# Optimization experiments

Hardware: AMD Instinct MI355X
Metric: run time of the kernel (lower is better)

The kernel has to match this reference:

```python
import jax, jax.numpy as jnp
import numpy as np

EMBED_DIM = 2048
NUM_HEADS = 16
NUM_HEADS_KV = 16
HEAD_DIM = EMBED_DIM // NUM_HEADS  # 128
ROT_DIM = HEAD_DIM // 2            # rotary_emb_dim = 64 (partial rotary)
ROPE_BASE = 10000.0
SEQLEN = 2048


def _rope_cos_sin(seqlen):
    # inv_freq over rotary dim (fp32 positions, as pos_idx_in_fp32=True)
    inv_freq = 1.0 / (ROPE_BASE ** (jnp.arange(0, ROT_DIM, 2, dtype=jnp.float32) / ROT_DIM))
    t = jnp.arange(seqlen, dtype=jnp.float32)
    freqs = jnp.outer(t, inv_freq)                 # (S, ROT_DIM//2)
    return jnp.cos(freqs), jnp.sin(freqs)


def _apply_rotary(x, cos, sin):
    # x: (B, S, H, D); non-interleaved (GPT-NeoX) rotary on first ROT_DIM dims
    rd = cos.shape[-1] * 2
    x_rot, x_pass = x[..., :rd], x[..., rd:]
    x1, x2 = x_rot[..., : rd // 2], x_rot[..., rd // 2 :]
    c = cos[None, :, None, :]
    s = sin[None, :, None, :]
    o1 = x1 * c - x2 * s
    o2 = x1 * s + x2 * c
    return jnp.concatenate([o1, o2, x_pass], axis=-1)


def setup_inputs() -> dict:
    key = jax.random.key(0)
    ks = jax.random.split(key, 5)
    scale_in = 1.0 / np.sqrt(EMBED_DIM)
    return {
        "x_q": jax.random.normal(ks[0], (SEQLEN, EMBED_DIM), dtype=jnp.float32),
        "Wqkv_w": jax.random.normal(ks[1], (HEAD_DIM * (NUM_HEADS + 2 * NUM_HEADS_KV), EMBED_DIM), dtype=jnp.float32) * scale_in,
        "Wqkv_b": jax.random.normal(ks[2], (HEAD_DIM * (NUM_HEADS + 2 * NUM_HEADS_KV),), dtype=jnp.float32) * 0.01,
        "Wo_w": jax.random.normal(ks[3], (EMBED_DIM, EMBED_DIM), dtype=jnp.float32) * scale_in,
        "Wo_b": jax.random.normal(ks[4], (EMBED_DIM,), dtype=jnp.float32) * 0.01,
    }


def reference(x_q, Wqkv_w, Wqkv_b, Wo_w, Wo_b):
    S = x_q.shape[0]
    H, Hkv, D = NUM_HEADS, NUM_HEADS_KV, HEAD_DIM
    # fused QKV projection
    qkv = x_q @ Wqkv_w.T + Wqkv_b                     # (S, (H+2Hkv)*D)
    q = qkv[:, : H * D].reshape(1, S, H, D)
    kv = qkv[:, H * D :].reshape(1, S, 2, Hkv, D)
    # rotary (q_position_ids = k_position_ids = arange(S))
    cos, sin = _rope_cos_sin(S)
    q = _apply_rotary(q, cos, sin)
    k = _apply_rotary(kv[:, :, 0], cos, sin)          # (1, S, Hkv, D)
    v = kv[:, :, 1]
    # causal attention, softmax scale 1/sqrt(D)
    scores = jnp.einsum("bshd,bthd->bhst", q, k) / jnp.sqrt(jnp.float32(D))
    causal = jnp.arange(S)[:, None] >= jnp.arange(S)[None, :]  # (S, S)
    scores = jnp.where(causal[None, None], scores, jnp.float32(-1e30))
    attn = jax.nn.softmax(scores, axis=-1)
    out = jnp.einsum("bhst,bthd->bshd", attn, v)      # (1, S, H, D)
    out = out.reshape(1, S, H * D)
    out = out @ Wo_w.T + Wo_b
    return out[0]                                     # (S, E)
```

## Files before the change

kernel.cpp:

```cpp
#include <hip/hip_runtime.h>
#include <stdint.h>

#define QKV_N 6144
#define ATT_SCALE 0.08838834764831845f

typedef __attribute__((ext_vector_type(8))) short short8;
typedef __attribute__((ext_vector_type(4))) float f32x4;

__device__ __forceinline__ uint16_t f2b(float x){
  uint32_t u = __float_as_uint(x);
  uint32_t r = (u + 0x7fffu + ((u >> 16) & 1u)) >> 16;
  return (uint16_t)r;
}
__device__ __forceinline__ float b2f(uint16_t h){
  return __uint_as_float(((uint32_t)h) << 16);
}
__device__ __forceinline__ void g2l16(const void* g, void* l){
  __builtin_amdgcn_global_load_lds((const __attribute__((address_space(1))) void*)g,
                                   (__attribute__((address_space(3))) void*)l, 16, 0, 0);
}

__device__ __forceinline__ void cvt8(const float* __restrict__ in, uint16_t* __restrict__ out, int i){
  const float4* p = (const float4*)in;
  float4 a = p[2*i], b = p[2*i+1];
  union { short8 v; uint16_t u[8]; } o;
  o.u[0]=f2b(a.x); o.u[1]=f2b(a.y); o.u[2]=f2b(a.z); o.u[3]=f2b(a.w);
  o.u[4]=f2b(b.x); o.u[5]=f2b(b.y); o.u[6]=f2b(b.z); o.u[7]=f2b(b.w);
  ((short8*)out)[i] = o.v;
}

__global__ __launch_bounds__(256) void k_prep(const float* __restrict__ x,
                                              const float* __restrict__ wqkv,
                                              const float* __restrict__ wo,
                                              uint16_t* __restrict__ xb,
                                              uint16_t* __restrict__ wqkvb,
                                              uint16_t* __restrict__ wob,
                                              float* __restrict__ ct,
                                              float* __restrict__ st){
  const int b = blockIdx.x, tid = threadIdx.x;
  if (b < 2048) {
    cvt8(x, xb, b*256 + tid);
  } else if (b < 8192) {
    cvt8(wqkv, wqkvb, (b - 2048)*256 + tid);
  } else if (b < 10240) {
    cvt8(wo, wob, (b - 8192)*256 + tid);
  } else {
    int i = (b - 10240)*256 + tid;
    int s = i >> 5, d = i & 31;
    float inv = __expf(-(float)d * (9.210340371976184f / 32.0f));
    float f = (float)s * inv;
    ct[i] = cosf(f);
    st[i] = sinf(f);
  }
}

__global__ __launch_bounds__(512, 1) void k_gemmA(const uint16_t* __restrict__ A,
                                                  const uint16_t* __restrict__ B,
                                                  const float* __restrict__ bias,
                                                  uint16_t* __restrict__ C){
  __shared__ uint16_t As[3*4096];
  __shared__ uint16_t Bs[3*6144];
  const int K = 2048, N = 6144;

  const int wg = blockIdx.x;
  const int xcd = wg & 7, bi = wg >> 3;
  const int m0 = (xcd*2 + (bi & 1)) * 128;
  const int n0 = (bi >> 1) * 192;

  const int tid = threadIdx.x;
  const int wid = tid >> 6, l = tid & 63;
  const int wm = wid >> 2, wn = wid & 3;
  const int g = l >> 4, c = l & 15;

  const int rpA = tid >> 3, sA = (tid & 7) ^ (rpA & 7);
  const size_t srcA0 = (size_t)(m0 + rpA*2 + (sA >> 2)) * K + (sA & 3) * 8;
  const size_t srcB0 = (size_t)(n0 + rpA*2 + (sA >> 2)) * K + (sA & 3) * 8;
  const int rpB2 = 64 + (tid >> 3), sB2 = (tid & 7) ^ (rpB2 & 7);
  const size_t srcB1 = (size_t)(n0 + rpB2*2 + (sB2 >> 2)) * K + (sB2 & 3) * 8;

  const int pg   = ((c & 1) << 2) | g;
  const int slb  = (pg ^ ((c >> 1) & 7)) << 3;
  const int rpa0 = wm*32 + (c >> 1);
  const int rpb0 = wn*24 + (c >> 1);

  f32x4 acc[4][3] = {};
  const int NT = K >> 5;

  #pragma unroll
  for (int t0 = 0; t0 < 2; ++t0) {
    g2l16(A + srcA0 + t0*32, (void*)(As + t0*4096 + tid*8));
    g2l16(B + srcB0 + t0*32, (void*)(Bs + t0*6144 + tid*8));
    if (tid < 256)
      g2l16(B + srcB1 + t0*32, (void*)(Bs + t0*6144 + 4096 + tid*8));
  }
  if (wid < 4) { asm volatile("s_waitcnt vmcnt(3)" ::: "memory"); }
  else         { asm volatile("s_waitcnt vmcnt(2)" ::: "memory"); }
  __builtin_amdgcn_s_barrier();

  #pragma unroll 3
  for (int t = 0; t < NT; ++t) {
    const uint16_t* __restrict__ Ab = As + (t % 3)*4096;
    const uint16_t* __restrict__ Bb = Bs + (t % 3)*6144;
    const int t2 = t + 2;

    short8 av[4], bv[3];
    #pragma unroll
    for (int mi = 0; mi < 4; ++mi)
      av[mi] = *(const short8*)&Ab[(rpa0 + mi*8)*64 + slb];
    #pragma unroll
    for (int ni = 0; ni < 3; ++ni)
      bv[ni] = *(const short8*)&Bb[(rpb0 + ni*8)*64 + slb];
    if (t2 < NT) {
      const int b2 = (t2 % 3);
      g2l16(A + srcA0 + t2*32, (void*)(As + b2*4096 + tid*8));
      g2l16(B + srcB0 + t2*32, (void*)(Bs + b2*6144 + tid*8));
      if (tid < 256)
        g2l16(B + srcB1 + t2*32, (void*)(Bs + b2*6144 + 4096 + tid*8));
    }
    __builtin_amdgcn_s_barrier();
    __builtin_amdgcn_s_setprio(1);
    #pragma unroll
    for (int mi = 0; mi < 4; ++mi)
      #pragma unroll
      for (int ni = 0; ni < 3; ++ni)
        acc[mi][ni] = __builtin_amdgcn_mfma_f32_16x16x32_bf16(av[mi], bv[ni], acc[mi][ni], 0, 0, 0);
    __builtin_amdgcn_s_setprio(0);
    if (wid < 4) { asm volatile("s_waitcnt vmcnt(3)" ::: "memory"); }
    else         { asm volatile("s_waitcnt vmcnt(2)" ::: "memory"); }
    __builtin_amdgcn_s_barrier();
  }

  #pragma unroll
  for (int ni = 0; ni < 3; ++ni) {
    const int col = n0 + wn*48 + ni*16 + c;
    const float bvl = bias[col];
    #pragma unroll
    for (int mi = 0; mi < 4; ++mi) {
      const int row0 = m0 + wm*64 + mi*16 + g*4;
      #pragma unroll
      for (int j = 0; j < 4; ++j)
        C[(size_t)(row0 + j)*N + col] = f2b(acc[mi][ni][j] + bvl);
    }
  }
}

__global__ __launch_bounds__(512, 1) void k_gemm128(const uint16_t* __restrict__ A,
                                                    const uint16_t* __restrict__ B,
                                                    const float* __restrict__ bias,
                                                    float* __restrict__ C,
                                                    int M, int N, int K){
  __shared__ uint16_t As[4*4096];
  __shared__ uint16_t Bs[4*4096];

  const int wg = blockIdx.x;
  const int xcd = wg & 7, bi = wg >> 3;
  const int m0 = (xcd*2 + (bi & 1)) * 128;
  const int n0 = (bi >> 1) * 128;

  const int tid = threadIdx.x;
  const int wid = tid >> 6, l = tid & 63;
  const int wm = wid >> 2, wn = wid & 3;
  const int g = l >> 4, c = l & 15;

  const int rp_s = tid >> 3, q_s = tid & 7, s_s = q_s ^ (rp_s & 7);
  const int srcA = (m0 + rp_s*2 + (s_s >> 2)) * K + (s_s & 3) * 8;
  const int srcB = (n0 + rp_s*2 + (s_s >> 2)) * K + (s_s & 3) * 8;

  const int pg  = ((c & 1) << 2) | g;
  const int slb = (pg ^ ((c >> 1) & 7)) << 3;
  const int ra0 = wm*32 + (c >> 1);
  const int rb0 = wn*16 + (c >> 1);

  f32x4 acc[4][2] = {};
  const int NT = K >> 5;

  #pragma unroll
  for (int t0 = 0; t0 < 3; ++t0) {
    g2l16(A + srcA + t0*32, (void*)(As + t0*4096 + tid*8));
    g2l16(B + srcB + t0*32, (void*)(Bs + t0*4096 + tid*8));
  }
  asm volatile("s_waitcnt vmcnt(4)" ::: "memory");
  __builtin_amdgcn_s_barrier();

  #pragma unroll 4
  for (int t = 0; t < NT; ++t) {
    const uint16_t* __restrict__ Ab = As + (t & 3)*4096;
    const uint16_t* __restrict__ Bb = Bs + (t & 3)*4096;
    const int t3 = t + 3;
    const int b3 = (t3 & 3)*4096;

    short8 av[4], bv[2];
    #pragma unroll
    for (int mi = 0; mi < 4; ++mi)
      av[mi] = *(const short8*)&Ab[(ra0 + mi*8)*64 + slb];
    #pragma unroll
    for (int ni = 0; ni < 2; ++ni)
      bv[ni] = *(const short8*)&Bb[(rb0 + ni*8)*64 + slb];
    if (t3 < NT) {
      g2l16(A + srcA + t3*32, (void*)(As + b3 + tid*8));
      g2l16(B + srcB + t3*32, (void*)(Bs + b3 + tid*8));
    }
    __builtin_amdgcn_s_barrier();
    __builtin_amdgcn_s_setprio(1);
    #pragma unroll
    for (int mi = 0; mi < 4; ++mi)
      #pragma unroll
      for (int ni = 0; ni < 2; ++ni)
        acc[mi][ni] = __builtin_amdgcn_mfma_f32_16x16x32_bf16(av[mi], bv[ni], acc[mi][ni], 0, 0, 0);
    __builtin_amdgcn_s_setprio(0);
    asm volatile("s_waitcnt vmcnt(4)" ::: "memory");
    __builtin_amdgcn_s_barrier();
  }

  #pragma unroll
  for (int ni = 0; ni < 2; ++ni) {
    const int col = n0 + wn*32 + ni*16 + c;
    const float bvl = bias[col];
    #pragma unroll
    for (int mi = 0; mi < 4; ++mi) {
      const int row0 = m0 + wm*64 + mi*16 + g*4;
      #pragma unroll
      for (int j = 0; j < 4; ++j)
        C[(size_t)(row0 + j)*N + col] = acc[mi][ni][j] + bvl;
    }
  }
}

__global__ __launch_bounds__(256) void k_rope_vt(const uint16_t* __restrict__ qkv,
                                                 const float* __restrict__ ct,
                                                 const float* __restrict__ st,
                                                 uint16_t* __restrict__ qo,
                                                 uint16_t* __restrict__ ko,
                                                 uint16_t* __restrict__ vt){
  const int blk = blockIdx.x, tid = threadIdx.x;
  if (blk < 4096) {
    int idx = blk * 256 + tid;
    int db = idx & 15;
    int s  = (idx >> 4) & 2047;
    int h  = (idx >> 15) & 15;
    int which = idx >> 19;
    const uint16_t* src = qkv + (size_t)s * QKV_N + which * 2048 + h * 128;
    uint16_t* dst = (which ? ko : qo) + (((size_t)(h*2048 + s)) << 7) + db*8;
    const float scale = which ? 1.0f : ATT_SCALE;
    int d0 = db * 8;
    union { short8 v; uint16_t u[8]; } o;
    if (d0 >= 64) {
      short8 xv = *(const short8*)(src + d0);
      #pragma unroll
      for (int e = 0; e < 8; ++e) o.u[e] = f2b(b2f((uint16_t)xv[e]) * scale);
    } else {
      int dd = d0 & 31;
      short8 a = *(const short8*)(src + dd);
      short8 b = *(const short8*)(src + dd + 32);
      float4 c0 = *(const float4*)(ct + s*32 + dd);
      float4 c1 = *(const float4*)(ct + s*32 + dd + 4);
      float4 s0 = *(const float4*)(st + s*32 + dd);
      float4 s1 = *(const float4*)(st + s*32 + dd + 4);
      float cc[8] = {c0.x,c0.y,c0.z,c0.w,c1.x,c1.y,c1.z,c1.w};
      float ss[8] = {s0.x,s0.y,s0.z,s0.w,s1.x,s1.y,s1.z,s1.w};
      #pragma unroll
      for (int e = 0; e < 8; ++e) {
        float x1 = b2f((uint16_t)a[e]), x2 = b2f((uint16_t)b[e]);
        float v = (d0 < 32) ? (x1*cc[e] - x2*ss[e]) : (x1*ss[e] + x2*cc[e]);
        o.u[e] = f2b(v * scale);
      }
    }
    *(short8*)dst = o.v;
  } else {
    __shared__ uint16_t tl[64][80];
    const int b = blk - 4096;
    const int st_ = b & 31, dt = (b >> 5) & 1, h = b >> 6;
    const int s_l = tid >> 2, cch = (tid & 3) * 16;
    const uint16_t* src = qkv + (size_t)(st_*64 + s_l) * QKV_N + 4096 + h*128 + dt*64 + cch;
    short8 a = *(const short8*)src;
    short8 b2 = *(const short8*)(src + 8);
    #pragma unroll
    for (int e = 0; e < 8; ++e) {
      tl[cch + e][s_l]     = (uint16_t)a[e];
      tl[cch + 8 + e][s_l] = (uint16_t)b2[e];
    }
    __syncthreads();
    const int d_l = tid >> 2;
    uint16_t* dst = vt + ((size_t)h << 18) + (size_t)(dt*64 + d_l) * 2048 + st_*64 + cch;
    *(short8*)dst       = *(const short8*)&tl[d_l][cch];
    *(short8*)(dst + 8) = *(const short8*)&tl[d_l][cch + 8];
  }
}

__global__ __launch_bounds__(512, 1) void k_attn(const uint16_t* __restrict__ Q,
                                                 const uint16_t* __restrict__ Kb,
                                                 const uint16_t* __restrict__ Vtg,
                                                 uint16_t* __restrict__ Out){
  __shared__ uint16_t Ks[2][2][64*128];
  __shared__ uint16_t Vs[2][2][128*64];
  __shared__ uint16_t Ps[8][16*88];

  const int bid = blockIdx.x;
  const int lin = (bid & 7) * 32 + (bid >> 3);
  const int h = lin >> 4;
  const int pair = lin & 15;

  const int tid = threadIdx.x, w = tid >> 6, l = tid & 63;
  const int gid = w >> 2, wq = w & 3;
  const int tg = tid & 255;
  const int g = l >> 4, c = l & 15;
  const int swz = (c & 7) << 4;

  const uint16_t* __restrict__ Qh = Q   + ((size_t)h << 18);
  const uint16_t* __restrict__ Kh = Kb  + ((size_t)h << 18);
  const uint16_t* __restrict__ Vh = Vtg + ((size_t)h << 18);
  float* scratch = (float*)&Ks[0][0][0];

  int koff[4], voff[4];
  #pragma unroll
  for (int j = 0; j < 4; ++j) {
    int kr = j*16 + (tg >> 4);
    koff[j] = kr*128 + (((tg & 15) ^ (kr & 7)) << 3);
    int vd = j*32 + (tg >> 3);
    voff[j] = vd*2048 + (((tg & 7) ^ (vd & 7)) << 3);
  }

  uint16_t* KsG = &Ks[gid][0][0];
  uint16_t* VsG = &Vs[gid][0][0];

  #pragma unroll 1
  for (int half = 0; half < 2; ++half) {
    const int qt = half ? (31 - pair) : pair;
    const int nt = qt + 1;
    const int nsteps = (nt + 1) >> 1;
    const int qrow = qt*64 + wq*16 + c;

    short8 qf[4];
    #pragma unroll
    for (int t = 0; t < 4; ++t)
      qf[t] = *(const short8*)&Qh[(size_t)qrow*128 + t*32 + g*8];

    f32x4 acc[8] = {};
    float mrow[4], lsum[4];
    #pragma unroll
    for (int j = 0; j < 4; ++j) { mrow[j] = -3e38f; lsum[j] = 0.0f; }

    if (gid < nt) {
      #pragma unroll
      for (int j = 0; j < 4; ++j) {
        g2l16(Kh + (size_t)gid*8192 + koff[j], (void*)(KsG + j*2048 + tg*8));
        g2l16(Vh + gid*64 + voff[j],           (void*)(VsG + j*2048 + tg*8));
      }
    }
    asm volatile("s_waitcnt vmcnt(0)" ::: "memory");
    __syncthreads();

    #pragma unroll 1
    for (int step = 0; step < nsteps; ++step) {
      const int kt = 2*step + gid;
      const int cur = step & 1;
      if (kt + 2 < nt) {
        const int k1 = kt + 2;
        #pragma unroll
        for (int j = 0; j < 4; ++j) {
          g2l16(Kh + (size_t)k1*8192 + koff[j], (void*)(KsG + (cur^1)*8192 + j*2048 + tg*8));
          g2l16(Vh + k1*64 + voff[j],           (void*)(VsG + (cur^1)*8192 + j*2048 + tg*8));
        }
      }

      if (kt < nt) {
        const int k0 = kt * 64;
        const uint16_t* Kcur = KsG + cur*8192;
        const uint16_t* Vcur = VsG + cur*8192;

        f32x4 sc4[4] = {};
        __builtin_amdgcn_s_setprio(1);
        #pragma unroll
        for (int ct2 = 0; ct2 < 4; ++ct2) {
          const char* krp = (const char*)Kcur + (ct2*16 + c)*256;
          #pragma unroll
          for (int t = 0; t < 4; ++t) {
            short8 kb = *(const short8*)(krp + ((t*64 + g*16) ^ swz));
            sc4[ct2] = __builtin_amdgcn_mfma_f32_16x16x32_bf16(qf[t], kb, sc4[ct2], 0, 0, 0);
          }
        }
        __builtin_amdgcn_s_setprio(0);

        const bool lastt = (kt == nt - 1);
        float va[4][4];
        float m4[4];
        int fastok = 1;
        #pragma unroll
        for (int j = 0; j < 4; ++j) {
          const int qg = qt*64 + wq*16 + g*4 + j;
          float v0 = sc4[0][j], v1 = sc4[1][j], v2 = sc4[2][j], v3 = sc4[3][j];
          if (lastt) {
            if (k0 +      c > qg) v0 = -3e38f;
            if (k0 + 16 + c > qg) v1 = -3e38f;
            if (k0 + 32 + c > qg) v2 = -3e38f;
            if (k0 + 48 + c > qg) v3 = -3e38f;
          }
          va[j][0] = v0; va[j][1] = v1; va[j][2] = v2; va[j][3] = v3;
          float m = fmaxf(fmaxf(fmaxf(v0, v1), v2), v3);
          m4[j] = m;
          fastok &= (m <= mrow[j] + 8.0f) ? 1 : 0;
        }
        if (__all(fastok)) {
          #pragma unroll
          for (int j = 0; j < 4; ++j) {
            const float mj = mrow[j];
            const float p0 = __expf(va[j][0] - mj), p1 = __expf(va[j][1] - mj),
                        p2 = __expf(va[j][2] - mj), p3 = __expf(va[j][3] - mj);
            lsum[j] += (p0 + p1) + (p2 + p3);
            uint16_t* pw = &Ps[w][(g*4 + j)*88];
            pw[c] = f2b(p0); pw[16+c] = f2b(p1); pw[32+c] = f2b(p2); pw[48+c] = f2b(p3);
          }
        } else {
          #pragma unroll
          for (int j = 0; j < 4; ++j) {
            float t0 = m4[j];
            #pragma unroll
            for (int d2 = 1; d2 < 16; d2 <<= 1) t0 = fmaxf(t0, __shfl_xor(t0, d2, 64));
            const float mn = fmaxf(mrow[j], t0);
            const float scl = __expf(mrow[j] - mn);
            const float p0 = __expf(va[j][0] - mn), p1 = __expf(va[j][1] - mn),
                        p2 = __expf(va[j][2] - mn), p3 = __expf(va[j][3] - mn);
            lsum[j] = lsum[j]*scl + (p0 + p1) + (p2 + p3);
            mrow[j] = mn;
            #pragma unroll
            for (int n = 0; n < 8; ++n) acc[n][j] *= scl;
            uint16_t* pw = &Ps[w][(g*4 + j)*88];
            pw[c] = f2b(p0); pw[16+c] = f2b(p1); pw[32+c] = f2b(p2); pw[48+c] = f2b(p3);
          }
        }

        __builtin_amdgcn_s_setprio(1);
        #pragma unroll
        for (int kk = 0; kk < 2; ++kk) {
          short8 pf = *(const short8*)&Ps[w][c*88 + kk*32 + g*8];
          #pragma unroll
          for (int n = 0; n < 8; ++n) {
            const char* vrp = (const char*)Vcur + (n*16 + c)*128;
            short8 vf = *(const short8*)(vrp + ((kk*64 + g*16) ^ swz));
            acc[n] = __builtin_amdgcn_mfma_f32_16x16x32_bf16(pf, vf, acc[n], 0, 0, 0);
          }
        }
        __builtin_amdgcn_s_setprio(0);
      }

      asm volatile("s_waitcnt vmcnt(0)" ::: "memory");
      __syncthreads();
    }

    float lrow[4];
    #pragma unroll
    for (int j = 0; j < 4; ++j) {
      float rs = lsum[j];
      #pragma unroll
      for (int d2 = 1; d2 < 16; d2 <<= 1) rs += __shfl_xor(rs, d2, 64);
      lrow[j] = rs;
    }

    float* Up = scratch + wq * 2112;
    if (gid == 1) {
      #pragma unroll
      for (int j = 0; j < 4; ++j) {
        const int row = g*4 + j;
        #pragma unroll
        for (int n = 0; n < 8; ++n)
          Up[row*128 + n*16 + c] = acc[n][j];
        if (c == 0) { Up[2048 + row] = mrow[j]; Up[2064 + row] = lrow[j]; }
      }
    }
    __syncthreads();
    if (gid == 0) {
      #pragma unroll
      for (int j = 0; j < 4; ++j) {
        const int row = g*4 + j;
        const int qg = qt*64 + wq*16 + row;
        const float mB = Up[2048 + row], lB = Up[2064 + row];
        const float mn = fmaxf(mrow[j], mB);
        const float e1 = __expf(mrow[j] - mn);
        const float e2 = __expf(mB - mn);
        const float inv = 1.0f / (lrow[j]*e1 + lB*e2);
        #pragma unroll
        for (int n = 0; n < 8; ++n) {
          const float u = acc[n][j]*e1 + Up[row*128 + n*16 + c]*e2;
          Out[(size_t)qg*2048 + h*128 + n*16 + c] = f2b(u * inv);
        }
      }
    }
    __syncthreads();
  }
}

extern "C" void kernel_launch(void* const* d_in, const int* in_sizes, int n_in,
                              void* d_out, int out_size, void* d_ws, size_t ws_size,
                              hipStream_t stream){
  const float* x    = (const float*)d_in[0];
  const float* Wqkv = (const float*)d_in[1];
  const float* bqkv = (const float*)d_in[2];
  const float* Wo   = (const float*)d_in[3];
  const float* bo   = (const float*)d_in[4];

  char* ws = (char*)d_ws;
  uint16_t* q_bf    = (uint16_t*)(ws);
  uint16_t* k_bf    = (uint16_t*)(ws + 8388608);
  uint16_t* vt_bf   = (uint16_t*)(ws + 16777216);
  uint16_t* attn_bf = (uint16_t*)(ws + 25165824);
  uint16_t* x_bf    = attn_bf;
  uint16_t* wqkv_bf = (uint16_t*)(ws + 33554432);
  uint16_t* wo_bf   = (uint16_t*)(ws + 58720256);
  uint16_t* qkv_bf  = (uint16_t*)(ws + 67108864);
  float*    cos_t   = (float*)(ws + 92274688);
  float*    sin_t   = (float*)(ws + 92536832);

  k_prep<<<dim3(10496), dim3(256), 0, stream>>>(x, Wqkv, Wo, x_bf, wqkv_bf, wo_bf,
                                                cos_t, sin_t);
  k_gemmA<<<dim3(512), dim3(512), 0, stream>>>(x_bf, wqkv_bf, bqkv, qkv_bf);
  k_rope_vt<<<dim3(5120), dim3(256), 0, stream>>>(qkv_bf, cos_t, sin_t, q_bf, k_bf, vt_bf);
  k_attn<<<dim3(256), dim3(512), 0, stream>>>(q_bf, k_bf, vt_bf, attn_bf);
  k_gemm128<<<dim3(256), dim3(512), 0, stream>>>(attn_bf, wo_bf, bo, (float*)d_out,
                                                 2048, 2048, 2048);
}
```

Measured before the change: 165.2 us.

## Enlarge QKV GEMM tiles to 256x256 with quadrant-split double-buffered pipeline

```diff
diff --git a/kernel.cpp b/kernel.cpp
--- a/kernel.cpp
+++ b/kernel.cpp
@@ -58,85 +58,150 @@
                                                   const uint16_t* __restrict__ B,
                                                   const float* __restrict__ bias,
                                                   uint16_t* __restrict__ C){
-  __shared__ uint16_t As[3*4096];
-  __shared__ uint16_t Bs[3*6144];
+  __shared__ uint16_t As[2*16384];
+  __shared__ uint16_t Bs[2*16384];
   const int K = 2048, N = 6144;
 
   const int wg = blockIdx.x;
-  const int xcd = wg & 7, bi = wg >> 3;
-  const int m0 = (xcd*2 + (bi & 1)) * 128;
-  const int n0 = (bi >> 1) * 192;
+  const int xcd = wg & 7, ib = wg >> 3;
+  const int m0 = (ib / 3) * 256;
+  const int n0 = (xcd * 3 + (ib % 3)) * 256;
 
   const int tid = threadIdx.x;
   const int wid = tid >> 6, l = tid & 63;
   const int wm = wid >> 2, wn = wid & 3;
   const int g = l >> 4, c = l & 15;
 
-  const int rpA = tid >> 3, sA = (tid & 7) ^ (rpA & 7);
-  const size_t srcA0 = (size_t)(m0 + rpA*2 + (sA >> 2)) * K + (sA & 3) * 8;
-  const size_t srcB0 = (size_t)(n0 + rpA*2 + (sA >> 2)) * K + (sA & 3) * 8;
-  const int rpB2 = 64 + (tid >> 3), sB2 = (tid & 7) ^ (rpB2 & 7);
-  const size_t srcB1 = (size_t)(n0 + rpB2*2 + (sB2 >> 2)) * K + (sB2 & 3) * 8;
-
-  const int pg   = ((c & 1) << 2) | g;
-  const int slb  = (pg ^ ((c >> 1) & 7)) << 3;
-  const int rpa0 = wm*32 + (c >> 1);
-  const int rpb0 = wn*24 + (c >> 1);
-
-  f32x4 acc[4][3] = {};
-  const int NT = K >> 5;
-
+  const int srow = tid >> 3, sq = tid & 7;
+  const int scol = (sq ^ (srow & 7)) * 8;
+  size_t srcA[2][2], srcB[2][2];
   #pragma unroll
-  for (int t0 = 0; t0 < 2; ++t0) {
-    g2l16(A + srcA0 + t0*32, (void*)(As + t0*4096 + tid*8));
-    g2l16(B + srcB0 + t0*32, (void*)(Bs + t0*6144 + tid*8));
-    if (tid < 256)
-      g2l16(B + srcB1 + t0*32, (void*)(Bs + t0*6144 + 4096 + tid*8));
-  }
-  if (wid < 4) { asm volatile("s_waitcnt vmcnt(3)" ::: "memory"); }
-  else         { asm volatile("s_waitcnt vmcnt(2)" ::: "memory"); }
+  for (int hf = 0; hf < 2; ++hf)
+    #pragma unroll
+    for (int r = 0; r < 2; ++r) {
+      srcA[hf][r] = (size_t)(m0 + hf*128 + r*64 + srow) * K + scol;
+      srcB[hf][r] = (size_t)(n0 + hf*128 + r*64 + srow) * K + scol;
+    }
+
+  const int sl0 = ((g)     ^ (c & 7)) << 3;
+  const int sl1 = ((4 | g) ^ (c & 7)) << 3;
+  const int arb = (wm*128 + c) * 64;
+  const int brb = (wn*64  + c) * 64;
+
+  f32x4 acc[8][4] = {};
+  const int NT = K >> 6;
+
+  #pragma unroll
+  for (int t0 = 0; t0 < 2; ++t0)
+    #pragma unroll
+    for (int hf = 0; hf < 2; ++hf)
+      #pragma unroll
+      for (int r = 0; r < 2; ++r) {
+        g2l16(A + srcA[hf][r] + t0*64, (void*)(As + t0*16384 + hf*8192 + r*4096 + tid*8));
+        g2l16(B + srcB[hf][r] + t0*64, (void*)(Bs + t0*16384 + hf*8192 + r*4096 + tid*8));
+      }
+  asm volatile("s_waitcnt vmcnt(8)" ::: "memory");
   __builtin_amdgcn_s_barrier();
 
-  #pragma unroll 3
   for (int t = 0; t < NT; ++t) {
-    const uint16_t* __restrict__ Ab = As + (t % 3)*4096;
-    const uint16_t* __restrict__ Bb = Bs + (t % 3)*6144;
-    const int t2 = t + 2;
-
-    short8 av[4], bv[3];
+    const int cur = t & 1;
+    const uint16_t* __restrict__ Ab = As + cur*16384;
+    const uint16_t* __restrict__ Bb = Bs + cur*16384;
+    const bool pf = (t + 2) < NT;
+    const size_t ko = (size_t)(t + 2) * 64;
+    short8 a1[8], b0[4], b1[4], a2[8];
+
+    #pragma unroll
+    for (int mi = 0; mi < 4; ++mi) {
+      a1[mi*2]   = *(const short8*)&Ab[arb + mi*1024 + sl0];
+      a1[mi*2+1] = *(const short8*)&Ab[arb + mi*1024 + sl1];
+    }
+    #pragma unroll
+    for (int ni = 0; ni < 2; ++ni) {
+      b0[ni*2]   = *(const short8*)&Bb[brb + ni*1024 + sl0];
+      b0[ni*2+1] = *(const short8*)&Bb[brb + ni*1024 + sl1];
+    }
+    __builtin_amdgcn_s_barrier();
+    __builtin_amdgcn_s_setprio(1);
     #pragma unroll
     for (int mi = 0; mi < 4; ++mi)
-      av[mi] = *(const short8*)&Ab[(rpa0 + mi*8)*64 + slb];
-    #pragma unroll
-    for (int ni = 0; ni < 3; ++ni)
-      bv[ni] = *(const short8*)&Bb[(rpb0 + ni*8)*64 + slb];
-    if (t2 < NT) {
-      const int b2 = (t2 % 3);
-      g2l16(A + srcA0 + t2*32, (void*)(As + b2*4096 + tid*8));
-      g2l16(B + srcB0 + t2*32, (void*)(Bs + b2*6144 + tid*8));
-      if (tid < 256)
-        g2l16(B + srcB1 + t2*32, (void*)(Bs + b2*6144 + 4096 + tid*8));
+      #pragma unroll
+      for (int ni = 0; ni < 2; ++ni)
+        #pragma unroll
+        for (int kk = 0; kk < 2; ++kk)
+          acc[mi][ni] = __builtin_amdgcn_mfma_f32_16x16x32_bf16(a1[mi*2+kk], b0[ni*2+kk], acc[mi][ni], 0, 0, 0);
+    __builtin_amdgcn_s_setprio(0);
+    __builtin_amdgcn_s_barrier();
+
+    #pragma unroll
+    for (int ni = 0; ni < 2; ++ni) {
+      b1[ni*2]   = *(const short8*)&Bb[brb + (ni+2)*1024 + sl0];
+      b1[ni*2+1] = *(const short8*)&Bb[brb + (ni+2)*1024 + sl1];
     }
     __builtin_amdgcn_s_barrier();
     __builtin_amdgcn_s_setprio(1);
     #pragma unroll
     for (int mi = 0; mi < 4; ++mi)
       #pragma unroll
-      for (int ni = 0; ni < 3; ++ni)
-        acc[mi][ni] = __builtin_amdgcn_mfma_f32_16x16x32_bf16(av[mi], bv[ni], acc[mi][ni], 0, 0, 0);
+      for (int ni = 0; ni < 2; ++ni)
+        #pragma unroll
+        for (int kk = 0; kk < 2; ++kk)
+          acc[mi][ni+2] = __builtin_amdgcn_mfma_f32_16x16x32_bf16(a1[mi*2+kk], b1[ni*2+kk], acc[mi][ni+2], 0, 0, 0);
     __builtin_amdgcn_s_setprio(0);
-    if (wid < 4) { asm volatile("s_waitcnt vmcnt(3)" ::: "memory"); }
-    else         { asm volatile("s_waitcnt vmcnt(2)" ::: "memory"); }
+    __builtin_amdgcn_s_barrier();
+
+    if (pf) {
+      #pragma unroll
+      for (int hf = 0; hf < 2; ++hf)
+        #pragma unroll
+        for (int r = 0; r < 2; ++r)
+          g2l16(B + srcB[hf][r] + ko, (void*)(Bs + cur*16384 + hf*8192 + r*4096 + tid*8));
+    }
+    #pragma unroll
+    for (int mi = 0; mi < 4; ++mi) {
+      a2[mi*2]   = *(const short8*)&Ab[arb + (mi+4)*1024 + sl0];
+      a2[mi*2+1] = *(const short8*)&Ab[arb + (mi+4)*1024 + sl1];
+    }
+    __builtin_amdgcn_s_barrier();
+    __builtin_amdgcn_s_setprio(1);
+    #pragma unroll
+    for (int mi = 0; mi < 4; ++mi)
+      #pragma unroll
+      for (int ni = 0; ni < 2; ++ni)
+        #pragma unroll
+        for (int kk = 0; kk < 2; ++kk)
+          acc[mi+4][ni+2] = __builtin_amdgcn_mfma_f32_16x16x32_bf16(a2[mi*2+kk], b1[ni*2+kk], acc[mi+4][ni+2], 0, 0, 0);
+    __builtin_amdgcn_s_setprio(0);
+    __builtin_amdgcn_s_barrier();
+
+    if (pf) {
+      #pragma unroll
+      for (int hf = 0; hf < 2; ++hf)
+        #pragma unroll
+        for (int r = 0; r < 2; ++r)
+          g2l16(A + srcA[hf][r] + ko, (void*)(As + cur*16384 + hf*8192 + r*4096 + tid*8));
+    }
+    __builtin_amdgcn_s_setprio(1);
+    #pragma unroll
+    for (int mi = 0; mi < 4; ++mi)
+      #pragma unroll
+      for (int ni = 0; ni < 2; ++ni)
+        #pragma unroll
+        for (int kk = 0; kk < 2; ++kk)
+          acc[mi+4][ni] = __builtin_amdgcn_mfma_f32_16x16x32_bf16(a2[mi*2+kk], b0[ni*2+kk], acc[mi+4][ni], 0, 0, 0);
+    __builtin_amdgcn_s_setprio(0);
+    if (pf) { asm volatile("s_waitcnt vmcnt(8)" ::: "memory"); }
+    else    { asm volatile("s_waitcnt vmcnt(0)" ::: "memory"); }
     __builtin_amdgcn_s_barrier();
   }
 
   #pragma unroll
-  for (int ni = 0; ni < 3; ++ni) {
-    const int col = n0 + wn*48 + ni*16 + c;
+  for (int ni = 0; ni < 4; ++ni) {
+    const int col = n0 + wn*64 + ni*16 + c;
     const float bvl = bias[col];
     #pragma unroll
-    for (int mi = 0; mi < 4; ++mi) {
-      const int row0 = m0 + wm*64 + mi*16 + g*4;
+    for (int mi = 0; mi < 8; ++mi) {
+      const int row0 = m0 + wm*128 + mi*16 + g*4;
       #pragma unroll
       for (int j = 0; j < 4; ++j)
         C[(size_t)(row0 + j)*N + col] = f2b(acc[mi][ni][j] + bvl);
@@ -512,7 +577,7 @@
 
   k_prep<<<dim3(10496), dim3(256), 0, stream>>>(x, Wqkv, Wo, x_bf, wqkv_bf, wo_bf,
                                                 cos_t, sin_t);
-  k_gemmA<<<dim3(512), dim3(512), 0, stream>>>(x_bf, wqkv_bf, bqkv, qkv_bf);
+  k_gemmA<<<dim3(192), dim3(512), 0, stream>>>(x_bf, wqkv_bf, bqkv, qkv_bf);
   k_rope_vt<<<dim3(5120), dim3(256), 0, stream>>>(qkv_bf, cos_t, sin_t, q_bf, k_bf, vt_bf);
   k_attn<<<dim3(256), dim3(512), 0, stream>>>(q_bf, k_bf, vt_bf, attn_bf);
   k_gemm128<<<dim3(256), dim3(512), 0, stream>>>(attn_bf, wo_bf, bo, (float*)d_out,
```

Result: no change. 165.9 us (+0.5%).

## Split attention into one block per query tile with 32-wide KV tiles

Applied to the files above, without the earlier changes.

```diff
diff --git a/kernel.cpp b/kernel.cpp
--- a/kernel.cpp
+++ b/kernel.cpp
@@ -287,18 +287,18 @@
   }
 }
 
-__global__ __launch_bounds__(512, 1) void k_attn(const uint16_t* __restrict__ Q,
+__global__ __launch_bounds__(512, 4) void k_attn(const uint16_t* __restrict__ Q,
                                                  const uint16_t* __restrict__ Kb,
                                                  const uint16_t* __restrict__ Vtg,
                                                  uint16_t* __restrict__ Out){
-  __shared__ uint16_t Ks[2][2][64*128];
-  __shared__ uint16_t Vs[2][2][128*64];
-  __shared__ uint16_t Ps[8][16*88];
+  __shared__ uint16_t Ks[2][2][32*128];
+  __shared__ uint16_t Vs[2][2][128*32];
+  __shared__ uint16_t Ps[8][16*40];
 
   const int bid = blockIdx.x;
-  const int lin = (bid & 7) * 32 + (bid >> 3);
-  const int h = lin >> 4;
-  const int pair = lin & 15;
+  const int xcd = bid & 7, r = bid >> 3;
+  const int h = 2*xcd + (r & 1);
+  const int qt = (r < 32) ? (r >> 1) : (31 - ((r - 32) >> 1));
 
   const int tid = threadIdx.x, w = tid >> 6, l = tid & 63;
   const int gid = w >> 2, wq = w & 3;
@@ -311,181 +311,166 @@
   const uint16_t* __restrict__ Vh = Vtg + ((size_t)h << 18);
   float* scratch = (float*)&Ks[0][0][0];
 
-  int koff[4], voff[4];
-  #pragma unroll
-  for (int j = 0; j < 4; ++j) {
+  int koff[2], voff[2];
+  #pragma unroll
+  for (int j = 0; j < 2; ++j) {
     int kr = j*16 + (tg >> 4);
     koff[j] = kr*128 + (((tg & 15) ^ (kr & 7)) << 3);
-    int vd = j*32 + (tg >> 3);
-    voff[j] = vd*2048 + (((tg & 7) ^ (vd & 7)) << 3);
+    int vd = j*64 + (tg >> 2);
+    voff[j] = vd*2048 + (((tg & 3) ^ (vd & 3)) << 3);
   }
 
   uint16_t* KsG = &Ks[gid][0][0];
   uint16_t* VsG = &Vs[gid][0][0];
 
+  const int nt = (qt + 1) * 2;
+  const int nsteps = nt >> 1;
+  const int qrow = qt*64 + wq*16 + c;
+
+  short8 qf[4];
+  #pragma unroll
+  for (int t = 0; t < 4; ++t)
+    qf[t] = *(const short8*)&Qh[(size_t)qrow*128 + t*32 + g*8];
+
+  f32x4 acc[8] = {};
+  float mrow[4], lsum[4];
+  #pragma unroll
+  for (int j = 0; j < 4; ++j) { mrow[j] = -3e38f; lsum[j] = 0.0f; }
+
+  #pragma unroll
+  for (int j = 0; j < 2; ++j) {
+    g2l16(Kh + (size_t)gid*4096 + koff[j], (void*)(KsG + j*2048 + tg*8));
+    g2l16(Vh + gid*32 + voff[j],           (void*)(VsG + j*2048 + tg*8));
+  }
+  asm volatile("s_waitcnt vmcnt(0)" ::: "memory");
+  __syncthreads();
+
   #pragma unroll 1
-  for (int half = 0; half < 2; ++half) {
-    const int qt = half ? (31 - pair) : pair;
-    const int nt = qt + 1;
-    const int nsteps = (nt + 1) >> 1;
-    const int qrow = qt*64 + wq*16 + c;
-
-    short8 qf[4];
-    #pragma unroll
-    for (int t = 0; t < 4; ++t)
-      qf[t] = *(const short8*)&Qh[(size_t)qrow*128 + t*32 + g*8];
-
-    f32x4 acc[8] = {};
-    float mrow[4], lsum[4];
-    #pragma unroll
-    for (int j = 0; j < 4; ++j) { mrow[j] = -3e38f; lsum[j] = 0.0f; }
-
-    if (gid < nt) {
+  for (int step = 0; step < nsteps; ++step) {
+    const int kt = 2*step + gid;
+    const int cur = step & 1;
+    if (kt + 2 < nt) {
+      const int k1 = kt + 2;
+      #pragma unroll
+      for (int j = 0; j < 2; ++j) {
+        g2l16(Kh + (size_t)k1*4096 + koff[j], (void*)(KsG + (cur^1)*4096 + j*2048 + tg*8));
+        g2l16(Vh + k1*32 + voff[j],           (void*)(VsG + (cur^1)*4096 + j*2048 + tg*8));
+      }
+    }
+
+    {
+      const int k0 = kt * 32;
+      const uint16_t* Kcur = KsG + cur*4096;
+      const uint16_t* Vcur = VsG + cur*4096;
+
+      f32x4 sc2[2] = {};
+      __builtin_amdgcn_s_setprio(1);
+      #pragma unroll
+      for (int ct2 = 0; ct2 < 2; ++ct2) {
+        const char* krp = (const char*)Kcur + (ct2*16 + c)*256;
+        #pragma unroll
+        for (int t = 0; t < 4; ++t) {
+          short8 kb = *(const short8*)(krp + ((t*64 + g*16) ^ swz));
+          sc2[ct2] = __builtin_amdgcn_mfma_f32_16x16x32_bf16(qf[t], kb, sc2[ct2], 0, 0, 0);
+        }
+      }
+      __builtin_amdgcn_s_setprio(0);
+
+      const bool maskt = (kt >= nt - 2);
+      float m4[4];
+      int fastok = 1;
       #pragma unroll
       for (int j = 0; j < 4; ++j) {
-        g2l16(Kh + (size_t)gid*8192 + koff[j], (void*)(KsG + j*2048 + tg*8));
-        g2l16(Vh + gid*64 + voff[j],           (void*)(VsG + j*2048 + tg*8));
-      }
-    }
+        const int qg = qt*64 + wq*16 + g*4 + j;
+        float v0 = sc2[0][j], v1 = sc2[1][j];
+        if (maskt) {
+          if (k0 +      c > qg) v0 = -3e38f;
+          if (k0 + 16 + c > qg) v1 = -3e38f;
+        }
+        sc2[0][j] = v0; sc2[1][j] = v1;
+        float m = fmaxf(v0, v1);
+        m4[j] = m;
+        fastok &= (m <= mrow[j] + 8.0f) ? 1 : 0;
+      }
+      if (__all(fastok)) {
+        #pragma unroll
+        for (int j = 0; j < 4; ++j) {
+          const float mj = mrow[j];
+          const float p0 = __expf(sc2[0][j] - mj), p1 = __expf(sc2[1][j] - mj);
+          lsum[j] += p0 + p1;
+          uint16_t* pw = &Ps[w][(g*4 + j)*40];
+          pw[c] = f2b(p0); pw[16+c] = f2b(p1);
+        }
+      } else {
+        #pragma unroll
+        for (int j = 0; j < 4; ++j) {
+          float t0 = m4[j];
+          #pragma unroll
+          for (int d2 = 1; d2 < 16; d2 <<= 1) t0 = fmaxf(t0, __shfl_xor(t0, d2, 64));
+          const float mn = fmaxf(mrow[j], t0);
+          const float scl = __expf(mrow[j] - mn);
+          const float p0 = __expf(sc2[0][j] - mn), p1 = __expf(sc2[1][j] - mn);
+          lsum[j] = lsum[j]*scl + p0 + p1;
+          mrow[j] = mn;
+          #pragma unroll
+          for (int n = 0; n < 8; ++n) acc[n][j] *= scl;
+          uint16_t* pw = &Ps[w][(g*4 + j)*40];
+          pw[c] = f2b(p0); pw[16+c] = f2b(p1);
+        }
+      }
+
+      short8 pf = *(const short8*)&Ps[w][c*40 + g*8];
+      __builtin_amdgcn_s_setprio(1);
+      #pragma unroll
+      for (int n = 0; n < 8; ++n) {
+        const char* vrp = (const char*)Vcur + (n*16 + c)*64;
+        short8 vf = *(const short8*)(vrp + ((g*16) ^ (((c & 3)) << 4)));
+        acc[n] = __builtin_amdgcn_mfma_f32_16x16x32_bf16(pf, vf, acc[n], 0, 0, 0);
+      }
+      __builtin_amdgcn_s_setprio(0);
+    }
+
     asm volatile("s_waitcnt vmcnt(0)" ::: "memory");
     __syncthreads();
-
-    #pragma unroll 1
-    for (int step = 0; step < nsteps; ++step) {
-      const int kt = 2*step + gid;
-      const int cur = step & 1;
-      if (kt + 2 < nt) {
-        const int k1 = kt + 2;
-        #pragma unroll
-        for (int j = 0; j < 4; ++j) {
-          g2l16(Kh + (size_t)k1*8192 + koff[j], (void*)(KsG + (cur^1)*8192 + j*2048 + tg*8));
-          g2l16(Vh + k1*64 + voff[j],           (void*)(VsG + (cur^1)*8192 + j*2048 + tg*8));
-        }
-      }
-
-      if (kt < nt) {
-        const int k0 = kt * 64;
-        const uint16_t* Kcur = KsG + cur*8192;
-        const uint16_t* Vcur = VsG + cur*8192;
-
-        f32x4 sc4[4] = {};
-        __builtin_amdgcn_s_setprio(1);
-        #pragma unroll
-        for (int ct2 = 0; ct2 < 4; ++ct2) {
-          const char* krp = (const char*)Kcur + (ct2*16 + c)*256;
-          #pragma unroll
-          for (int t = 0; t < 4; ++t) {
-            short8 kb = *(const short8*)(krp + ((t*64 + g*16) ^ swz));
-            sc4[ct2] = __builtin_amdgcn_mfma_f32_16x16x32_bf16(qf[t], kb, sc4[ct2], 0, 0, 0);
-          }
-        }
-        __builtin_amdgcn_s_setprio(0);
-
-        const bool lastt = (kt == nt - 1);
-        float va[4][4];
-        float m4[4];
-        int fastok = 1;
-        #pragma unroll
-        for (int j = 0; j < 4; ++j) {
-          const int qg = qt*64 + wq*16 + g*4 + j;
-          float v0 = sc4[0][j], v1 = sc4[1][j], v2 = sc4[2][j], v3 = sc4[3][j];
-          if (lastt) {
-            if (k0 +      c > qg) v0 = -3e38f;
-            if (k0 + 16 + c > qg) v1 = -3e38f;
-            if (k0 + 32 + c > qg) v2 = -3e38f;
-            if (k0 + 48 + c > qg) v3 = -3e38f;
-          }
-          va[j][0] = v0; va[j][1] = v1; va[j][2] = v2; va[j][3] = v3;
-          float m = fmaxf(fmaxf(fmaxf(v0, v1), v2), v3);
-          m4[j] = m;
-          fastok &= (m <= mrow[j] + 8.0f) ? 1 : 0;
-        }
-        if (__all(fastok)) {
-          #pragma unroll
-          for (int j = 0; j < 4; ++j) {
-            const float mj = mrow[j];
-            const float p0 = __expf(va[j][0] - mj), p1 = __expf(va[j][1] - mj),
-                        p2 = __expf(va[j][2] - mj), p3 = __expf(va[j][3] - mj);
-            lsum[j] += (p0 + p1) + (p2 + p3);
-            uint16_t* pw = &Ps[w][(g*4 + j)*88];
-            pw[c] = f2b(p0); pw[16+c] = f2b(p1); pw[32+c] = f2b(p2); pw[48+c] = f2b(p3);
-          }
-        } else {
-          #pragma unroll
-          for (int j = 0; j < 4; ++j) {
-            float t0 = m4[j];
-            #pragma unroll
-            for (int d2 = 1; d2 < 16; d2 <<= 1) t0 = fmaxf(t0, __shfl_xor(t0, d2, 64));
-            const float mn = fmaxf(mrow[j], t0);
-            const float scl = __expf(mrow[j] - mn);
-            const float p0 = __expf(va[j][0] - mn), p1 = __expf(va[j][1] - mn),
-                        p2 = __expf(va[j][2] - mn), p3 = __expf(va[j][3] - mn);
-            lsum[j] = lsum[j]*scl + (p0 + p1) + (p2 + p3);
-            mrow[j] = mn;
-            #pragma unroll
-            for (int n = 0; n < 8; ++n) acc[n][j] *= scl;
-            uint16_t* pw = &Ps[w][(g*4 + j)*88];
-            pw[c] = f2b(p0); pw[16+c] = f2b(p1); pw[32+c] = f2b(p2); pw[48+c] = f2b(p3);
-          }
-        }
-
-        __builtin_amdgcn_s_setprio(1);
-        #pragma unroll
-        for (int kk = 0; kk < 2; ++kk) {
-          short8 pf = *(const short8*)&Ps[w][c*88 + kk*32 + g*8];
-          #pragma unroll
-          for (int n = 0; n < 8; ++n) {
-            const char* vrp = (const char*)Vcur + (n*16 + c)*128;
-            short8 vf = *(const short8*)(vrp + ((kk*64 + g*16) ^ swz));
-            acc[n] = __builtin_amdgcn_mfma_f32_16x16x32_bf16(pf, vf, acc[n], 0, 0, 0);
-          }
-        }
-        __builtin_amdgcn_s_setprio(0);
-      }
-
-      asm volatile("s_waitcnt vmcnt(0)" ::: "memory");
-      __syncthreads();
-    }
-
-    float lrow[4];
+  }
+
+  float lrow[4];
+  #pragma unroll
+  for (int j = 0; j < 4; ++j) {
+    float rs = lsum[j];
+    #pragma unroll
+    for (int d2 = 1; d2 < 16; d2 <<= 1) rs += __shfl_xor(rs, d2, 64);
+    lrow[j] = rs;
+  }
+
+  float* Up = scratch + wq * 2112;
+  if (gid == 1) {
     #pragma unroll
     for (int j = 0; j < 4; ++j) {
-      float rs = lsum[j];
-      #pragma unroll
-      for (int d2 = 1; d2 < 16; d2 <<= 1) rs += __shfl_xor(rs, d2, 64);
-      lrow[j] = rs;
-    }
-
-    float* Up = scratch + wq * 2112;
-    if (gid == 1) {
-      #pragma unroll
-      for (int j = 0; j < 4; ++j) {
-        const int row = g*4 + j;
-        #pragma unroll
-        for (int n = 0; n < 8; ++n)
-          Up[row*128 + n*16 + c] = acc[n][j];
-        if (c == 0) { Up[2048 + row] = mrow[j]; Up[2064 + row] = lrow[j]; }
-      }
-    }
-    __syncthreads();
-    if (gid == 0) {
-      #pragma unroll
-      for (int j = 0; j < 4; ++j) {
-        const int row = g*4 + j;
-        const int qg = qt*64 + wq*16 + row;
-        const float mB = Up[2048 + row], lB = Up[2064 + row];
-        const float mn = fmaxf(mrow[j], mB);
-        const float e1 = __expf(mrow[j] - mn);
-        const float e2 = __expf(mB - mn);
-        const float inv = 1.0f / (lrow[j]*e1 + lB*e2);
-        #pragma unroll
-        for (int n = 0; n < 8; ++n) {
-          const float u = acc[n][j]*e1 + Up[row*128 + n*16 + c]*e2;
-          Out[(size_t)qg*2048 + h*128 + n*16 + c] = f2b(u * inv);
-        }
-      }
-    }
-    __syncthreads();
+      const int row = g*4 + j;
+      #pragma unroll
+      for (int n = 0; n < 8; ++n)
+        Up[row*128 + n*16 + c] = acc[n][j];
+      if (c == 0) { Up[2048 + row] = mrow[j]; Up[2064 + row] = lrow[j]; }
+    }
+  }
+  __syncthreads();
+  if (gid == 0) {
+    #pragma unroll
+    for (int j = 0; j < 4; ++j) {
+      const int row = g*4 + j;
+      const int qg = qt*64 + wq*16 + row;
+      const float mB = Up[2048 + row], lB = Up[2064 + row];
+      const float mn = fmaxf(mrow[j], mB);
+      const float e1 = __expf(mrow[j] - mn);
+      const float e2 = __expf(mB - mn);
+      const float inv = 1.0f / (lrow[j]*e1 + lB*e2);
+      #pragma unroll
+      for (int n = 0; n < 8; ++n) {
+        const float u = acc[n][j]*e1 + Up[row*128 + n*16 + c]*e2;
+        Out[(size_t)qg*2048 + h*128 + n*16 + c] = f2b(u * inv);
+      }
+    }
   }
 }
 
@@ -514,7 +499,7 @@
                                                 cos_t, sin_t);
   k_gemmA<<<dim3(512), dim3(512), 0, stream>>>(x_bf, wqkv_bf, bqkv, qkv_bf);
   k_rope_vt<<<dim3(5120), dim3(256), 0, stream>>>(qkv_bf, cos_t, sin_t, q_bf, k_bf, vt_bf);
-  k_attn<<<dim3(256), dim3(512), 0, stream>>>(q_bf, k_bf, vt_bf, attn_bf);
+  k_attn<<<dim3(512), dim3(512), 0, stream>>>(q_bf, k_bf, vt_bf, attn_bf);
   k_gemm128<<<dim3(256), dim3(512), 0, stream>>>(attn_bf, wo_bf, bo, (float*)d_out,
                                                  2048, 2048, 2048);
 }
```

After: 206.4 us. 25.0% more time.

## Rework QKV GEMM to 6 waves with 32x32x16 MFMA tiles

Applied to the files above, without the earlier changes.

```diff
diff --git a/kernel.cpp b/kernel.cpp
--- a/kernel.cpp
+++ b/kernel.cpp
@@ -6,6 +6,7 @@
 
 typedef __attribute__((ext_vector_type(8))) short short8;
 typedef __attribute__((ext_vector_type(4))) float f32x4;
+typedef __attribute__((ext_vector_type(16))) float f32x16;
 
 __device__ __forceinline__ uint16_t f2b(float x){
   uint32_t u = __float_as_uint(x);
@@ -54,12 +55,11 @@
   }
 }
 
-__global__ __launch_bounds__(512, 1) void k_gemmA(const uint16_t* __restrict__ A,
+__global__ __launch_bounds__(384, 1) void k_gemmA(const uint16_t* __restrict__ A,
                                                   const uint16_t* __restrict__ B,
                                                   const float* __restrict__ bias,
                                                   uint16_t* __restrict__ C){
-  __shared__ uint16_t As[3*4096];
-  __shared__ uint16_t Bs[3*6144];
+  __shared__ uint16_t Ls[3*10240];
   const int K = 2048, N = 6144;
 
   const int wg = blockIdx.x;
@@ -69,77 +69,100 @@
 
   const int tid = threadIdx.x;
   const int wid = tid >> 6, l = tid & 63;
-  const int wm = wid >> 2, wn = wid & 3;
-  const int g = l >> 4, c = l & 15;
-
-  const int rpA = tid >> 3, sA = (tid & 7) ^ (rpA & 7);
-  const size_t srcA0 = (size_t)(m0 + rpA*2 + (sA >> 2)) * K + (sA & 3) * 8;
-  const size_t srcB0 = (size_t)(n0 + rpA*2 + (sA >> 2)) * K + (sA & 3) * 8;
-  const int rpB2 = 64 + (tid >> 3), sB2 = (tid & 7) ^ (rpB2 & 7);
-  const size_t srcB1 = (size_t)(n0 + rpB2*2 + (sB2 >> 2)) * K + (sB2 & 3) * 8;
-
-  const int pg   = ((c & 1) << 2) | g;
-  const int slb  = (pg ^ ((c >> 1) & 7)) << 3;
-  const int rpa0 = wm*32 + (c >> 1);
-  const int rpb0 = wn*24 + (c >> 1);
-
-  f32x4 acc[4][3] = {};
+  const int wm = wid / 3, wn = wid % 3;
+  const int r31 = l & 31, h = l >> 5;
+
+  const uint16_t* gp[4];
+  int ldst[4];
+  #pragma unroll
+  for (int j = 0; j < 4; ++j) {
+    int f = (j < 3) ? (tid + 384*j) : (1152 + (tid & 127));
+    int isA = f < 512;
+    int fr = isA ? f : f - 512;
+    int rp = fr >> 3, q = fr & 7;
+    int s = q ^ (rp & 7);
+    int base = isA ? m0 : n0;
+    gp[j] = (isA ? A : B) + (size_t)(base + rp*2 + (s >> 2)) * K + (s & 3) * 8;
+    ldst[j] = (isA ? 0 : 4096) + fr*8;
+  }
+
+  const int rsw = (r31 >> 1) & 7;
+  const int wp4 = (r31 & 1) * 4;
+  const int arow = (wm*32 + (r31 >> 1)) * 64;
+  const int brow = 4096 + (wn*32 + (r31 >> 1)) * 64;
+
+  f32x16 acc[2][2] = {};
   const int NT = K >> 5;
 
   #pragma unroll
   for (int t0 = 0; t0 < 2; ++t0) {
-    g2l16(A + srcA0 + t0*32, (void*)(As + t0*4096 + tid*8));
-    g2l16(B + srcB0 + t0*32, (void*)(Bs + t0*6144 + tid*8));
-    if (tid < 256)
-      g2l16(B + srcB1 + t0*32, (void*)(Bs + t0*6144 + 4096 + tid*8));
-  }
-  if (wid < 4) { asm volatile("s_waitcnt vmcnt(3)" ::: "memory"); }
-  else         { asm volatile("s_waitcnt vmcnt(2)" ::: "memory"); }
+    g2l16(gp[0] + t0*32, (void*)(Ls + t0*10240 + ldst[0]));
+    g2l16(gp[1] + t0*32, (void*)(Ls + t0*10240 + ldst[1]));
+    g2l16(gp[2] + t0*32, (void*)(Ls + t0*10240 + ldst[2]));
+    if (tid < 128)
+      g2l16(gp[3] + t0*32, (void*)(Ls + t0*10240 + ldst[3]));
+  }
+  if (tid < 128) { asm volatile("s_waitcnt vmcnt(4)" ::: "memory"); }
+  else           { asm volatile("s_waitcnt vmcnt(3)" ::: "memory"); }
   __builtin_amdgcn_s_barrier();
 
   #pragma unroll 3
   for (int t = 0; t < NT; ++t) {
-    const uint16_t* __restrict__ Ab = As + (t % 3)*4096;
-    const uint16_t* __restrict__ Bb = Bs + (t % 3)*6144;
+    const uint16_t* __restrict__ Lb = Ls + (t % 3) * 10240;
     const int t2 = t + 2;
-
-    short8 av[4], bv[3];
-    #pragma unroll
-    for (int mi = 0; mi < 4; ++mi)
-      av[mi] = *(const short8*)&Ab[(rpa0 + mi*8)*64 + slb];
-    #pragma unroll
-    for (int ni = 0; ni < 3; ++ni)
-      bv[ni] = *(const short8*)&Bb[(rpb0 + ni*8)*64 + slb];
-    if (t2 < NT) {
-      const int b2 = (t2 % 3);
-      g2l16(A + srcA0 + t2*32, (void*)(As + b2*4096 + tid*8));
-      g2l16(B + srcB0 + t2*32, (void*)(Bs + b2*6144 + tid*8));
-      if (tid < 256)
-        g2l16(B + srcB1 + t2*32, (void*)(Bs + b2*6144 + 4096 + tid*8));
+    const bool pf = t2 < NT;
+
+    short8 a[2][2], b[2][2];
+    #pragma unroll
+    for (int mi = 0; mi < 2; ++mi)
+      #pragma unroll
+      for (int kk = 0; kk < 2; ++kk)
+        a[mi][kk] = *(const short8*)&Lb[arow + mi*1024 + ((wp4 + kk*2 + h) ^ rsw)*8];
+    #pragma unroll
+    for (int ni = 0; ni < 2; ++ni)
+      #pragma unroll
+      for (int kk = 0; kk < 2; ++kk)
+        b[ni][kk] = *(const short8*)&Lb[brow + ni*1024 + ((wp4 + kk*2 + h) ^ rsw)*8];
+
+    if (pf) {
+      const int bb = (t2 % 3) * 10240;
+      g2l16(gp[0] + t2*32, (void*)(Ls + bb + ldst[0]));
+      g2l16(gp[1] + t2*32, (void*)(Ls + bb + ldst[1]));
+      g2l16(gp[2] + t2*32, (void*)(Ls + bb + ldst[2]));
+      if (tid < 128)
+        g2l16(gp[3] + t2*32, (void*)(Ls + bb + ldst[3]));
     }
     __builtin_amdgcn_s_barrier();
     __builtin_amdgcn_s_setprio(1);
     #pragma unroll
-    for (int mi = 0; mi < 4; ++mi)
-      #pragma unroll
-      for (int ni = 0; ni < 3; ++ni)
-        acc[mi][ni] = __builtin_amdgcn_mfma_f32_16x16x32_bf16(av[mi], bv[ni], acc[mi][ni], 0, 0, 0);
+    for (int mi = 0; mi < 2; ++mi)
+      #pragma unroll
+      for (int ni = 0; ni < 2; ++ni)
+        #pragma unroll
+        for (int kk = 0; kk < 2; ++kk)
+          acc[mi][ni] = __builtin_amdgcn_mfma_f32_32x32x16_bf16(a[mi][kk], b[ni][kk], acc[mi][ni], 0, 0, 0);
     __builtin_amdgcn_s_setprio(0);
-    if (wid < 4) { asm volatile("s_waitcnt vmcnt(3)" ::: "memory"); }
-    else         { asm volatile("s_waitcnt vmcnt(2)" ::: "memory"); }
+    if (pf) {
+      if (tid < 128) { asm volatile("s_waitcnt vmcnt(4)" ::: "memory"); }
+      else           { asm volatile("s_waitcnt vmcnt(3)" ::: "memory"); }
+    } else {
+      asm volatile("s_waitcnt vmcnt(0)" ::: "memory");
+    }
     __builtin_amdgcn_s_barrier();
   }
 
   #pragma unroll
-  for (int ni = 0; ni < 3; ++ni) {
-    const int col = n0 + wn*48 + ni*16 + c;
+  for (int ni = 0; ni < 2; ++ni) {
+    const int col = n0 + wn*64 + ni*32 + r31;
     const float bvl = bias[col];
     #pragma unroll
-    for (int mi = 0; mi < 4; ++mi) {
-      const int row0 = m0 + wm*64 + mi*16 + g*4;
-      #pragma unroll
-      for (int j = 0; j < 4; ++j)
-        C[(size_t)(row0 + j)*N + col] = f2b(acc[mi][ni][j] + bvl);
+    for (int mi = 0; mi < 2; ++mi) {
+      const int rowb = m0 + wm*64 + mi*32 + 4*h;
+      #pragma unroll
+      for (int reg = 0; reg < 16; ++reg) {
+        const int row = rowb + (reg & 3) + 8*(reg >> 2);
+        C[(size_t)row*N + col] = f2b(acc[mi][ni][reg] + bvl);
+      }
     }
   }
 }
@@ -512,7 +535,7 @@
 
   k_prep<<<dim3(10496), dim3(256), 0, stream>>>(x, Wqkv, Wo, x_bf, wqkv_bf, wo_bf,
                                                 cos_t, sin_t);
-  k_gemmA<<<dim3(512), dim3(512), 0, stream>>>(x_bf, wqkv_bf, bqkv, qkv_bf);
+  k_gemmA<<<dim3(512), dim3(384), 0, stream>>>(x_bf, wqkv_bf, bqkv, qkv_bf);
   k_rope_vt<<<dim3(5120), dim3(256), 0, stream>>>(qkv_bf, cos_t, sin_t, q_bf, k_bf, vt_bf);
   k_attn<<<dim3(256), dim3(512), 0, stream>>>(q_bf, k_bf, vt_bf, attn_bf);
   k_gemm128<<<dim3(256), dim3(512), 0, stream>>>(attn_bf, wo_bf, bo, (float*)d_out,
```

Measured after the change: 169.8 us. +2.8%, slower.
